# Kernel optimization log

Measured on AMD Instinct MI355X. Metric: run time of the kernel, lower is better.

## Reference

```python
import jax, jax.numpy as jnp
import numpy as np

B, T, IN, HID, BR, OUT = 128, 250, 700, 1024, 4, 20
VTH1, VTH2, DT = 0.5, 0.5, 1.0

# heaviside spike with multi-gaussian surrogate grad (DH-SNN ActFun_adp)
@jax.custom_vjp
def spike_fn(v):
    return (v > 0).astype(v.dtype)

def _spike_fwd(v):
    return spike_fn(v), v

def _spike_bwd(v, g):
    gamma, lens, scale, hight = 0.5, 0.5, 6.0, 0.15
    def gauss(x, mu, sigma):
        return jnp.exp(-((x - mu) ** 2) / (2.0 * sigma ** 2)) / (jnp.sqrt(2.0 * jnp.pi) * sigma)
    sg = (gauss(v, 0.0, lens) * (1.0 + hight)
          - gauss(v, lens, scale * lens) * hight
          - gauss(v, -lens, scale * lens) * hight)
    return (g * sg * gamma,)

spike_fn.defvjp(_spike_fwd, _spike_bwd)

def _make_mask(rng):
    # each output neuron's BR branches see disjoint equal slices of a random permutation
    K = IN + HID  # pad == 0 since (IN+HID) % BR == 0
    seg = K // BR
    mask = np.zeros((HID * BR, K), dtype=np.int32)
    for i in range(HID):
        seq = rng.permutation(K)
        for j in range(BR):
            mask[i * BR + j, seq[j * seg:(j + 1) * seg]] = 1
    return mask

def setup_inputs() -> dict:
    key = jax.random.key(0)
    ks = jax.random.split(key, 10)
    K = IN + HID
    x = jax.random.uniform(ks[0], (B, T, IN), dtype=jnp.float32)
    W1 = jax.random.normal(ks[1], (HID * BR, K), dtype=jnp.float32) / jnp.sqrt(jnp.float32(K))
    b1 = jnp.zeros((HID * BR,), jnp.float32)
    tau_m1 = jax.random.uniform(ks[2], (HID,), jnp.float32, 0.0, 4.0)
    tau_n = jax.random.uniform(ks[3], (HID, BR), jnp.float32, 0.0, 4.0)
    W2 = jax.random.normal(ks[4], (OUT, HID), dtype=jnp.float32) / jnp.sqrt(jnp.float32(HID))
    b2 = jnp.zeros((OUT,), jnp.float32)
    tau_m2 = jax.random.uniform(ks[5], (OUT,), jnp.float32, 0.0, 4.0)
    mem1_0 = jax.random.uniform(ks[6], (B, HID), jnp.float32)
    mem2_0 = jax.random.uniform(ks[7], (B, OUT), jnp.float32)
    mask = jnp.asarray(_make_mask(np.random.default_rng(0)))
    return dict(x=x, W1=W1, b1=b1, tau_m1=tau_m1, tau_n=tau_n, W2=W2, b2=b2,
                tau_m2=tau_m2, mem1_0=mem1_0, mem2_0=mem2_0, mask=mask)

def reference(x, W1, b1, tau_m1, tau_n, W2, b2, tau_m2, mem1_0, mem2_0, mask):
    bsz = x.shape[0]
    W1m = W1 * mask.astype(W1.dtype)  # branch-sparse dendritic weights
    alpha1 = jax.nn.sigmoid(tau_m1)   # [HID]
    beta = jax.nn.sigmoid(tau_n)      # [HID, BR]
    alpha2 = jax.nn.sigmoid(tau_m2)   # [OUT]
    spk1_0 = jnp.zeros((bsz, HID), x.dtype)
    d0 = jnp.zeros((bsz, HID, BR), x.dtype)
    spk2_0 = jnp.zeros((bsz, OUT), x.dtype)

    def step(carry, x_t):
        mem1, spk1, d_inp, mem2, spk2 = carry
        k_in = jnp.concatenate([x_t, spk1], axis=1)          # [B, IN+HID]
        ff = (k_in @ W1m.T + b1).reshape(bsz, HID, BR)       # dendritic branch input
        d_inp = beta * d_inp + (1.0 - beta) * ff             # per-branch decay
        l_in = d_inp.sum(axis=2)                             # [B, HID]
        mem1 = mem1 * alpha1 + (1.0 - alpha1) * l_in - VTH1 * spk1 * DT
        spk1 = spike_fn(mem1 - VTH1)
        d2 = spk1 @ W2.T + b2
        mem2 = mem2 * alpha2 + (1.0 - alpha2) * d2 - VTH2 * spk2 * DT
        spk2 = spike_fn(mem2 - VTH2)
        out = jax.nn.log_softmax(mem2, axis=1)
        return (mem1, spk1, d_inp, mem2, spk2), out

    _, ys = jax.lax.scan(step, (mem1_0, spk1_0, d0, mem2_0, spk2_0), jnp.swapaxes(x, 0, 1))
    return jnp.transpose(ys, (1, 2, 0))  # [B, OUT, T]
```

## Files before the change

kernel.cpp:

```cpp
#include <hip/hip_runtime.h>
#include <stdint.h>

#define BATCH 128
#define TSTEPS 250
#define NIN 700
#define NHID 1024
#define NBR 4
#define NOUT 20
#define KDIM 1724
#define NR 4096
#define VTH 0.5f

typedef float f32x4 __attribute__((ext_vector_type(4)));
typedef short s16x8 __attribute__((ext_vector_type(8)));


__global__ void setup_small(const float* __restrict__ tau_m1, const float* __restrict__ tau_n,
                            const float* __restrict__ tau_m2, const float* __restrict__ W2,
                            float* __restrict__ alpha1, float* __restrict__ beta,
                            float* __restrict__ alpha2, float* __restrict__ W2T) {
    int i = blockIdx.x * blockDim.x + threadIdx.x;
    if (i < NHID)  alpha1[i] = 1.f / (1.f + expf(-tau_m1[i]));
    if (i < NR)    beta[i]   = 1.f / (1.f + expf(-tau_n[i]));
    if (i < 32)    alpha2[i] = (i < NOUT) ? 1.f / (1.f + expf(-tau_m2[i])) : 0.f;
    if (i < NHID * 32) {
        int j = i >> 5, o = i & 31;
        W2T[i] = (o < NOUT) ? W2[o * NHID + j] : 0.f;
    }
}

__device__ __forceinline__ uint16_t f2bf_rne(float x) {
    uint32_t u = __float_as_uint(x);
    return (uint16_t)((u + 0x7FFFu + ((u >> 16) & 1u)) >> 16);
}

__global__ void setup_weights(const float* __restrict__ W1, const int* __restrict__ mask,
                              float* __restrict__ W1xT, uint16_t* __restrict__ fragH,
                              uint16_t* __restrict__ fragL) {
    const int total1 = NIN * NR;
    const int total2 = 128 << 15;
    for (int i = blockIdx.x * blockDim.x + threadIdx.x; i < total1 + total2;
         i += gridDim.x * blockDim.x) {
        if (i < total1) {
            int k = i >> 12, r = i & 4095;
            size_t src = (size_t)r * KDIM + k;
            W1xT[i] = W1[src] * (float)mask[src];
        } else {
            int e = i - total1;
            int j = e & 7, lane = (e >> 3) & 63, ks = (e >> 9) & 31;
            int nt2 = (e >> 14) & 1, gb = e >> 15;
            int k = ks * 32 + ((lane >> 4) & 3) * 8 + j;
            int r = gb * 32 + nt2 * 16 + (lane & 15);
            size_t src = (size_t)r * KDIM + NIN + k;
            float w = W1[src] * (float)mask[src];
            uint16_t hb = f2bf_rne(w);
            float hf = __uint_as_float((uint32_t)hb << 16);
            fragH[e] = hb;
            fragL[e] = f2bf_rne(w - hf);
        }
    }
}

__global__ void init_state(const float* __restrict__ mem1_0, const float* __restrict__ mem2_0,
                           float* __restrict__ mem1, float* __restrict__ mem2,
                           float* __restrict__ spk2, float* __restrict__ d_inp,
                           uint32_t* __restrict__ spkg, uint32_t* __restrict__ bar) {
    int i = blockIdx.x * blockDim.x + threadIdx.x;
    if (i < BATCH * NR) d_inp[i] = 0.f;
    if (i < BATCH * NHID) mem1[i] = mem1_0[i];
    if (i < BATCH * NOUT) { mem2[i] = mem2_0[i]; spk2[i] = 0.f; }
    if (i < 8192) spkg[i] = 0u;
    if (i < 2048) bar[i] = 0u;
}


#define GBM 128
#define GBN 128
#define GBK 16

__global__ __launch_bounds__(256) void ffx_gemm(const float* __restrict__ x,
                                                const float* __restrict__ W1xT,
                                                const float* __restrict__ b1,
                                                float* __restrict__ ffx, int t0) {
    __shared__ float As[GBK][GBM];
    __shared__ float Bs[GBK][GBN];
    int dt = blockIdx.x, bn = blockIdx.y;
    int tid = threadIdx.x;
    int tn = tid & 15, tm = tid >> 4;

    float acc[8][8];
#pragma unroll
    for (int i = 0; i < 8; ++i)
#pragma unroll
        for (int j = 0; j < 8; ++j) acc[i][j] = 0.f;

    int m_l = tid >> 1;
    const float* xrow = x + ((size_t)m_l * TSTEPS + t0 + dt) * NIN;
    int kh = (tid & 1) * 8;
    int kb = tid >> 4;
    int nb = (tid & 15) * 8;

    for (int k0 = 0; k0 < NIN; k0 += GBK) {
        float av[8];
#pragma unroll
        for (int u = 0; u < 8; ++u) {
            int k = k0 + kh + u;
            av[u] = (k < NIN) ? xrow[k] : 0.f;
        }
#pragma unroll
        for (int u = 0; u < 8; ++u) As[kh + u][m_l] = av[u];

        bool kok = (k0 + kb) < NIN;
        const float* bp = W1xT + (size_t)(k0 + kb) * NR + bn * GBN + nb;
        float bv[8];
#pragma unroll
        for (int u = 0; u < 8; ++u) bv[u] = kok ? bp[u] : 0.f;
#pragma unroll
        for (int u = 0; u < 8; ++u) Bs[kb][nb + u] = bv[u];

        __syncthreads();
#pragma unroll
        for (int kk = 0; kk < GBK; ++kk) {
            float a[8], b[8];
#pragma unroll
            for (int u = 0; u < 8; ++u) a[u] = As[kk][tm * 8 + u];
#pragma unroll
            for (int u = 0; u < 8; ++u) b[u] = Bs[kk][tn * 8 + u];
#pragma unroll
            for (int i = 0; i < 8; ++i)
#pragma unroll
                for (int j = 0; j < 8; ++j) acc[i][j] += a[i] * b[j];
        }
        __syncthreads();
    }

    float bias[8];
#pragma unroll
    for (int j = 0; j < 8; ++j) bias[j] = b1[bn * GBN + tn * 8 + j];
#pragma unroll
    for (int i = 0; i < 8; ++i) {
        int brow = tm * 8 + i;
        float* cp = ffx + ((size_t)dt * BATCH + brow) * NR + bn * GBN + tn * 8;
#pragma unroll
        for (int j = 0; j < 8; ++j) cp[j] = acc[i][j] + bias[j];
    }
}


__global__ __launch_bounds__(512) void persist9(
    const float* __restrict__ alpha1, const float* __restrict__ beta,
    const float* __restrict__ alpha2, float* __restrict__ mem1,
    float* __restrict__ mem2, float* __restrict__ spk2,
    float* __restrict__ d_inp, const uint16_t* __restrict__ fragH_g,
    const uint16_t* __restrict__ fragL_g, const float* __restrict__ W2T,
    const float* __restrict__ ffx, const float* __restrict__ b2v,
    float* __restrict__ out, uint32_t* __restrict__ spkg,
    uint32_t* __restrict__ bar, int t0, int tc, int last, int epoch0) {
    __shared__ __align__(16) uint16_t lds_fh[32768];
    __shared__ __align__(16) uint16_t lds_fl[32768];
    __shared__ uint32_t lds_raw[2048];
    __shared__ uint32_t lds_mask[64 * 33];
    __shared__ float lds_part[2560];

    const int blk = blockIdx.x;
    const int tid = threadIdx.x;
    const int G   = blk >> 7;
    const int gb  = blk & 127;
    const int l   = tid & 63;
    const int wv  = tid >> 6;

    {
        const float4* sH = (const float4*)(fragH_g + (size_t)gb * 32768);
        const float4* sL = (const float4*)(fragL_g + (size_t)gb * 32768);
        for (int i4 = tid; i4 < 4096; i4 += 512) {
            ((float4*)lds_fh)[i4] = sH[i4];
            ((float4*)lds_fl)[i4] = sL[i4];
        }
    }

    const int mt  = wv >> 1;
    const int nt2 = wv & 1;
    const int arow = mt * 16 + (l & 15);
    const int ksl  = ((l >> 4) & 3) * 8;

    const int ub = tid >> 3;
    const int un = tid & 7;
    const int bg_ = G * 64 + ub;
    const int n_g = gb * 8 + un;
    const int r0  = gb * 32 + un * 4;
    const f32x4 bet = *(const f32x4*)&beta[r0];
    const float al  = alpha1[n_g];
    f32x4 di = *(const f32x4*)&d_inp[(size_t)bg_ * NR + r0];
    float mm = mem1[bg_ * NHID + n_g];

    const int o2 = tid & 31;
    const int sub = tid >> 5;
    const bool l2blk = (gb < 16) && ((sub & 3) == 0);
    const int b2l = gb * 4 + (sub >> 2);
    const int b2g = G * 64 + b2l;
    float m2 = 0.f, s2v = 0.f, a2 = 0.f, bo = 0.f;
    if (l2blk && o2 < NOUT) {
        a2 = alpha2[o2];
        bo = b2v[o2];
        m2 = mem2[b2g * NOUT + o2];
        s2v = spk2[b2g * NOUT + o2];
    }

    uint32_t* breg = bar + (size_t)G * 1024;
    const int sg = gb & 7;
    uint32_t* grpcnt = &breg[32 * (1 + sg)];
    uint32_t* goline = &breg[32 * (9 + sg)];
    const bool leader = (gb >= 120);

    const int iters = tc + (last ? 1 : 0);
    for (int it = 0; it < iters; ++it) {
        const int tt = t0 + it;

        f32x4 ff = {0.f, 0.f, 0.f, 0.f};
        if (tt < TSTEPS)
            ff = *(const f32x4*)(ffx + (size_t)it * (BATCH * NR) + (size_t)bg_ * NR + r0);

        if (it > 0) {
            if (tid == 0) {
                uint32_t tgt = (uint32_t)(epoch0 + it);
                if (leader) {
                    while (__hip_atomic_load(&breg[0], __ATOMIC_ACQUIRE,
                                             __HIP_MEMORY_SCOPE_AGENT) < 8u * tgt)
                        __builtin_amdgcn_s_sleep(2);
                    __hip_atomic_store(goline, tgt, __ATOMIC_RELEASE,
                                       __HIP_MEMORY_SCOPE_AGENT);
                } else {
                    while (__hip_atomic_load(goline, __ATOMIC_RELAXED,
                                             __HIP_MEMORY_SCOPE_AGENT) < tgt)
                        __builtin_amdgcn_s_sleep(2);
                }
            }
            __syncthreads();
        }

        {
            const uint32_t* spg = spkg + (size_t)((tt + 1) & 1) * 4096 + G * 2048;
#pragma unroll
            for (int k2 = 0; k2 < 4; ++k2) {
                int idx = tid + (k2 << 9);
                lds_raw[idx ^ ((idx >> 6) & 31)] =
                    __hip_atomic_load(&spg[idx], __ATOMIC_RELAXED, __HIP_MEMORY_SCOPE_AGENT);
            }
        }
        __syncthreads();

        {
#pragma unroll
            for (int k2 = 0; k2 < 4; ++k2) {
                int e = tid + (k2 << 9);
                int b = e >> 5, w = e & 31;
                uint32_t word = 0;
#pragma unroll
                for (int m = 0; m < 4; ++m) {
                    int raw = ((w << 2) + m) * 16 + (b >> 2);
                    uint32_t v = lds_raw[raw ^ ((raw >> 6) & 31)];
                    word |= ((v >> ((b & 3) * 8)) & 0xFFu) << (m * 8);
                }
                lds_mask[b * 33 + w] = word;
            }
        }
        __syncthreads();

        if (tt < TSTEPS) {
            f32x4 accH = {0.f, 0.f, 0.f, 0.f};
            f32x4 accL = {0.f, 0.f, 0.f, 0.f};
            const int maskbase = arow * 33;
            const int fbase = nt2 * 32;
#pragma unroll 4
            for (int ks = 0; ks < 32; ++ks) {
                uint32_t bits = (lds_mask[maskbase + ks] >> ksl) & 0xFFu;
                union { uint32_t u[4]; s16x8 v; } a;
                a.u[0] = ((bits & 1u)  ? 0x3F80u : 0u) | ((bits & 2u)   ? 0x3F800000u : 0u);
                a.u[1] = ((bits & 4u)  ? 0x3F80u : 0u) | ((bits & 8u)   ? 0x3F800000u : 0u);
                a.u[2] = ((bits & 16u) ? 0x3F80u : 0u) | ((bits & 32u)  ? 0x3F800000u : 0u);
                a.u[3] = ((bits & 64u) ? 0x3F80u : 0u) | ((bits & 128u) ? 0x3F800000u : 0u);
                const s16x8 bh = *(const s16x8*)&lds_fh[((fbase + ks) * 64 + l) * 8];
                const s16x8 bl = *(const s16x8*)&lds_fl[((fbase + ks) * 64 + l) * 8];
                accH = __builtin_amdgcn_mfma_f32_16x16x32_bf16(a.v, bh, accH, 0, 0, 0);
                accL = __builtin_amdgcn_mfma_f32_16x16x32_bf16(a.v, bl, accL, 0, 0, 0);
            }
            f32x4 d;
#pragma unroll
            for (int q = 0; q < 4; ++q) d[q] = accH[q] + accL[q];
            float* pp = lds_part + ((mt * 32 + nt2 * 16 + (l & 15)) * 20 + ((l >> 4) & 3) * 4);
            *(float4*)pp = *(float4*)&d;
        }
        __syncthreads();

        if (tt < TSTEPS) {
            const int rl0 = un * 4;
            float s[4];
#pragma unroll
            for (int q = 0; q < 4; ++q)
                s[q] = lds_part[((ub >> 4) * 32 + rl0 + q) * 20 + (ub & 15)];
#pragma unroll
            for (int q = 0; q < 4; ++q)
                di[q] = bet[q] * di[q] + (1.f - bet[q]) * (s[q] + ff[q]);
            float lsum = (di[0] + di[1]) + (di[2] + di[3]);
            float sp_prev = (float)((lds_mask[ub * 33 + (n_g >> 5)] >> (n_g & 31)) & 1u);
            float mn = mm * al + (1.f - al) * lsum - VTH * sp_prev;
            mm = mn;
            bool spk = (mn - VTH) > 0.f;
            unsigned long long bal = __ballot(spk);
            uint32_t* spn = spkg + (size_t)(tt & 1) * 4096 + G * 2048;
            if (l == 0)
                __hip_atomic_store(&spn[gb * 16 + wv * 2], (uint32_t)bal,
                                   __ATOMIC_RELAXED, __HIP_MEMORY_SCOPE_AGENT);
            if (l == 32)
                __hip_atomic_store(&spn[gb * 16 + wv * 2 + 1], (uint32_t)(bal >> 32),
                                   __ATOMIC_RELAXED, __HIP_MEMORY_SCOPE_AGENT);
        }

        __syncthreads();
        if (it + 1 < iters && tid == 0) {
            uint32_t e16 = 16u * (uint32_t)(epoch0 + it + 1);
            uint32_t old = __hip_atomic_fetch_add(grpcnt, 1u, __ATOMIC_RELEASE,
                                                  __HIP_MEMORY_SCOPE_AGENT);
            if (old == e16 - 1u)
                __hip_atomic_fetch_add(&breg[0], 1u, __ATOMIC_RELEASE,
                                       __HIP_MEMORY_SCOPE_AGENT);
        }

        if (tt > 0 && l2blk) {
            const uint32_t* mw = &lds_mask[b2l * 33];
            float d2 = bo;
            for (int w = 0; w < 32; ++w) {
                uint32_t bits = mw[w];
                while (bits) {
                    int p = __builtin_ctz(bits);
                    bits &= bits - 1;
                    d2 += W2T[(((w << 5) + p) << 5) + o2];
                }
            }
            float m2n = m2 * a2 + (1.f - a2) * d2 - VTH * s2v;
            m2 = m2n;
            s2v = ((m2n - VTH) > 0.f) ? 1.f : 0.f;
            float v = (o2 < NOUT) ? m2n : -3.4e38f;
#pragma unroll
            for (int off = 16; off >= 1; off >>= 1) v = fmaxf(v, __shfl_xor(v, off, 32));
            float e = (o2 < NOUT) ? expf(m2n - v) : 0.f;
            float ssum = e;
#pragma unroll
            for (int off = 16; off >= 1; off >>= 1) ssum += __shfl_xor(ssum, off, 32);
            if (o2 < NOUT) out[((size_t)b2g * NOUT + o2) * TSTEPS + (tt - 1)] = (m2n - v) - logf(ssum);
        }
    }

    *(f32x4*)&d_inp[(size_t)bg_ * NR + r0] = di;
    mem1[bg_ * NHID + n_g] = mm;
    if (l2blk && o2 < NOUT) {
        mem2[b2g * NOUT + o2] = m2;
        spk2[b2g * NOUT + o2] = s2v;
    }
}


extern "C" void kernel_launch(void* const* d_in, const int* in_sizes, int n_in,
                              void* d_out, int out_size, void* d_ws, size_t ws_size,
                              hipStream_t stream) {
    const float* x      = (const float*)d_in[0];
    const float* W1     = (const float*)d_in[1];
    const float* b1     = (const float*)d_in[2];
    const float* tau_m1 = (const float*)d_in[3];
    const float* tau_n  = (const float*)d_in[4];
    const float* W2     = (const float*)d_in[5];
    const float* b2     = (const float*)d_in[6];
    const float* tau_m2 = (const float*)d_in[7];
    const float* mem1_0 = (const float*)d_in[8];
    const float* mem2_0 = (const float*)d_in[9];
    const int*   mask   = (const int*)d_in[10];
    float* out = (float*)d_out;

    float* ws = (float*)d_ws;
    size_t F = 0;
    float* alpha1 = ws + F; F += 1024;
    float* beta   = ws + F; F += 4096;
    float* alpha2 = ws + F; F += 32;
    float* mem1   = ws + F; F += BATCH * NHID;
    float* mem2   = ws + F; F += BATCH * NOUT;
    float* spk2   = ws + F; F += BATCH * NOUT;
    float* d_inp  = ws + F; F += BATCH * NR;
    float* W1xT   = ws + F; F += (size_t)NIN * NR;
    uint16_t* fragH = (uint16_t*)(ws + F); F += (size_t)(128 << 15) / 2;
    uint16_t* fragL = (uint16_t*)(ws + F); F += (size_t)(128 << 15) / 2;
    float* W2T    = ws + F; F += NHID * 32;
    uint32_t* spkg = (uint32_t*)(ws + F); F += 8192;
    uint32_t* bar  = (uint32_t*)(ws + F); F += 2048;
    float* ffx = ws + F;

    size_t ws_f = ws_size / 4;
    size_t avail = (ws_f > F) ? (ws_f - F) : 0;
    size_t per_t = (size_t)BATCH * NR;
    int Tc = (int)(avail / per_t);
    if (Tc < 1) Tc = 1;
    if (Tc > TSTEPS) Tc = TSTEPS;

    hipLaunchKernelGGL(setup_small, dim3(128), dim3(256), 0, stream,
                       tau_m1, tau_n, tau_m2, W2, alpha1, beta, alpha2, W2T);
    hipLaunchKernelGGL(setup_weights, dim3(2048), dim3(256), 0, stream,
                       W1, mask, W1xT, fragH, fragL);
    hipLaunchKernelGGL(init_state, dim3(2048), dim3(256), 0, stream,
                       mem1_0, mem2_0, mem1, mem2, spk2, d_inp, spkg, bar);

    int chunk_start = 0;
    int barriers_done = 0;
    while (chunk_start < TSTEPS) {
        int tc = TSTEPS - chunk_start;
        if (tc > Tc) tc = Tc;
        int last = (chunk_start + tc >= TSTEPS) ? 1 : 0;

        hipLaunchKernelGGL(ffx_gemm, dim3(tc, 32), dim3(256), 0, stream,
                           x, W1xT, b1, ffx, chunk_start);
        hipLaunchKernelGGL(persist9, dim3(256), dim3(512), 0, stream,
                           alpha1, beta, alpha2, mem1, mem2, spk2, d_inp, fragH, fragL,
                           W2T, ffx, b2, out, spkg, bar, chunk_start, tc, last, barriers_done);

        int iters = tc + (last ? 1 : 0);
        barriers_done += iters - 1;
        chunk_start += tc;
    }
}
```

Baseline: 6.111 ms.

## Replace grid barrier with tagged 64-bit spike words polled per step

Removes the hierarchical atomic-counter grid barrier. Each spike word is now written together with a timestep tag in a 64-bit atomic store, using a 4-deep ring of buffers. Consumers spin on the tag of each word they need, so blocks synchronise only through data readiness instead of a counter plus leader broadcast. The LDS bit-transpose into a mask layout is also dropped, and the raw ballot layout is indexed directly in the MMA and output paths. This removes one barrier round trip per step, at the cost of doubling spike traffic and many threads polling global memory.

```diff
diff --git a/kernel.cpp b/kernel.cpp
--- a/kernel.cpp
+++ b/kernel.cpp
@@ -64,13 +64,12 @@
 __global__ void init_state(const float* __restrict__ mem1_0, const float* __restrict__ mem2_0,
                            float* __restrict__ mem1, float* __restrict__ mem2,
                            float* __restrict__ spk2, float* __restrict__ d_inp,
-                           uint32_t* __restrict__ spkg, uint32_t* __restrict__ bar) {
+                           uint32_t* __restrict__ spk) {
     int i = blockIdx.x * blockDim.x + threadIdx.x;
     if (i < BATCH * NR) d_inp[i] = 0.f;
     if (i < BATCH * NHID) mem1[i] = mem1_0[i];
     if (i < BATCH * NOUT) { mem2[i] = mem2_0[i]; spk2[i] = 0.f; }
-    if (i < 8192) spkg[i] = 0u;
-    if (i < 2048) bar[i] = 0u;
+    if (i < 32768) spk[i] = 0u;
 }
 
 
@@ -147,19 +146,18 @@
 }
 
 
-__global__ __launch_bounds__(512) void persist9(
+__global__ __launch_bounds__(512) void persist10(
     const float* __restrict__ alpha1, const float* __restrict__ beta,
     const float* __restrict__ alpha2, float* __restrict__ mem1,
     float* __restrict__ mem2, float* __restrict__ spk2,
     float* __restrict__ d_inp, const uint16_t* __restrict__ fragH_g,
     const uint16_t* __restrict__ fragL_g, const float* __restrict__ W2T,
     const float* __restrict__ ffx, const float* __restrict__ b2v,
-    float* __restrict__ out, uint32_t* __restrict__ spkg,
-    uint32_t* __restrict__ bar, int t0, int tc, int last, int epoch0) {
+    float* __restrict__ out, uint64_t* __restrict__ spk,
+    int t0, int tc, int last) {
     __shared__ __align__(16) uint16_t lds_fh[32768];
     __shared__ __align__(16) uint16_t lds_fl[32768];
     __shared__ uint32_t lds_raw[2048];
-    __shared__ uint32_t lds_mask[64 * 33];
     __shared__ float lds_part[2560];
 
     const int blk = blockIdx.x;
@@ -182,6 +180,9 @@
     const int nt2 = wv & 1;
     const int arow = mt * 16 + (l & 15);
     const int ksl  = ((l >> 4) & 3) * 8;
+    const int lhi  = (l >> 4) & 3;
+    const int rawoff = arow >> 2;
+    const int ashf   = (arow & 3) * 8;
 
     const int ub = tid >> 3;
     const int un = tid & 7;
@@ -206,12 +207,6 @@
         s2v = spk2[b2g * NOUT + o2];
     }
 
-    uint32_t* breg = bar + (size_t)G * 1024;
-    const int sg = gb & 7;
-    uint32_t* grpcnt = &breg[32 * (1 + sg)];
-    uint32_t* goline = &breg[32 * (9 + sg)];
-    const bool leader = (gb >= 120);
-
     const int iters = tc + (last ? 1 : 0);
     for (int it = 0; it < iters; ++it) {
         const int tt = t0 + it;
@@ -220,60 +215,37 @@
         if (tt < TSTEPS)
             ff = *(const f32x4*)(ffx + (size_t)it * (BATCH * NR) + (size_t)bg_ * NR + r0);
 
-        if (it > 0) {
-            if (tid == 0) {
-                uint32_t tgt = (uint32_t)(epoch0 + it);
-                if (leader) {
-                    while (__hip_atomic_load(&breg[0], __ATOMIC_ACQUIRE,
-                                             __HIP_MEMORY_SCOPE_AGENT) < 8u * tgt)
-                        __builtin_amdgcn_s_sleep(2);
-                    __hip_atomic_store(goline, tgt, __ATOMIC_RELEASE,
-                                       __HIP_MEMORY_SCOPE_AGENT);
-                } else {
-                    while (__hip_atomic_load(goline, __ATOMIC_RELAXED,
-                                             __HIP_MEMORY_SCOPE_AGENT) < tgt)
-                        __builtin_amdgcn_s_sleep(2);
+        __syncthreads();
+
+        {
+            const uint64_t* sp = spk + ((size_t)(tt & 3) * 2 + G) * 2048;
+            const uint32_t tag = (uint32_t)tt;
+            uint64_t v[4];
+#pragma unroll
+            for (int k2 = 0; k2 < 4; ++k2)
+                v[k2] = __hip_atomic_load(&sp[tid + (k2 << 9)], __ATOMIC_RELAXED,
+                                          __HIP_MEMORY_SCOPE_AGENT);
+#pragma unroll
+            for (int k2 = 0; k2 < 4; ++k2) {
+                while ((uint32_t)v[k2] != tag) {
+                    __builtin_amdgcn_s_sleep(1);
+                    v[k2] = __hip_atomic_load(&sp[tid + (k2 << 9)], __ATOMIC_RELAXED,
+                                              __HIP_MEMORY_SCOPE_AGENT);
                 }
             }
-            __syncthreads();
-        }
-
-        {
-            const uint32_t* spg = spkg + (size_t)((tt + 1) & 1) * 4096 + G * 2048;
-#pragma unroll
-            for (int k2 = 0; k2 < 4; ++k2) {
-                int idx = tid + (k2 << 9);
-                lds_raw[idx ^ ((idx >> 6) & 31)] =
-                    __hip_atomic_load(&spg[idx], __ATOMIC_RELAXED, __HIP_MEMORY_SCOPE_AGENT);
-            }
-        }
-        __syncthreads();
-
-        {
-#pragma unroll
-            for (int k2 = 0; k2 < 4; ++k2) {
-                int e = tid + (k2 << 9);
-                int b = e >> 5, w = e & 31;
-                uint32_t word = 0;
-#pragma unroll
-                for (int m = 0; m < 4; ++m) {
-                    int raw = ((w << 2) + m) * 16 + (b >> 2);
-                    uint32_t v = lds_raw[raw ^ ((raw >> 6) & 31)];
-                    word |= ((v >> ((b & 3) * 8)) & 0xFFu) << (m * 8);
-                }
-                lds_mask[b * 33 + w] = word;
-            }
+#pragma unroll
+            for (int k2 = 0; k2 < 4; ++k2)
+                lds_raw[tid + (k2 << 9)] = (uint32_t)(v[k2] >> 32);
         }
         __syncthreads();
 
         if (tt < TSTEPS) {
             f32x4 accH = {0.f, 0.f, 0.f, 0.f};
             f32x4 accL = {0.f, 0.f, 0.f, 0.f};
-            const int maskbase = arow * 33;
             const int fbase = nt2 * 32;
 #pragma unroll 4
             for (int ks = 0; ks < 32; ++ks) {
-                uint32_t bits = (lds_mask[maskbase + ks] >> ksl) & 0xFFu;
+                uint32_t bits = (lds_raw[((ks << 2) + lhi) * 16 + rawoff] >> ashf) & 0xFFu;
                 union { uint32_t u[4]; s16x8 v; } a;
                 a.u[0] = ((bits & 1u)  ? 0x3F80u : 0u) | ((bits & 2u)   ? 0x3F800000u : 0u);
                 a.u[1] = ((bits & 4u)  ? 0x3F80u : 0u) | ((bits & 8u)   ? 0x3F800000u : 0u);
@@ -302,39 +274,33 @@
             for (int q = 0; q < 4; ++q)
                 di[q] = bet[q] * di[q] + (1.f - bet[q]) * (s[q] + ff[q]);
             float lsum = (di[0] + di[1]) + (di[2] + di[3]);
-            float sp_prev = (float)((lds_mask[ub * 33 + (n_g >> 5)] >> (n_g & 31)) & 1u);
+            float sp_prev = (float)((lds_raw[gb * 16 + (ub >> 2)] >> ((ub & 3) * 8 + un)) & 1u);
             float mn = mm * al + (1.f - al) * lsum - VTH * sp_prev;
             mm = mn;
-            bool spk = (mn - VTH) > 0.f;
-            unsigned long long bal = __ballot(spk);
-            uint32_t* spn = spkg + (size_t)(tt & 1) * 4096 + G * 2048;
+            bool spkb = (mn - VTH) > 0.f;
+            unsigned long long bal = __ballot(spkb);
+            uint64_t* spn = spk + ((size_t)((tt + 1) & 3) * 2 + G) * 2048;
+            const uint64_t ntag = (uint64_t)(uint32_t)(tt + 1);
             if (l == 0)
-                __hip_atomic_store(&spn[gb * 16 + wv * 2], (uint32_t)bal,
+                __hip_atomic_store(&spn[gb * 16 + wv * 2],
+                                   ((uint64_t)(uint32_t)bal << 32) | ntag,
                                    __ATOMIC_RELAXED, __HIP_MEMORY_SCOPE_AGENT);
             if (l == 32)
-                __hip_atomic_store(&spn[gb * 16 + wv * 2 + 1], (uint32_t)(bal >> 32),
+                __hip_atomic_store(&spn[gb * 16 + wv * 2 + 1],
+                                   ((uint64_t)(uint32_t)(bal >> 32) << 32) | ntag,
                                    __ATOMIC_RELAXED, __HIP_MEMORY_SCOPE_AGENT);
         }
 
-        __syncthreads();
-        if (it + 1 < iters && tid == 0) {
-            uint32_t e16 = 16u * (uint32_t)(epoch0 + it + 1);
-            uint32_t old = __hip_atomic_fetch_add(grpcnt, 1u, __ATOMIC_RELEASE,
-                                                  __HIP_MEMORY_SCOPE_AGENT);
-            if (old == e16 - 1u)
-                __hip_atomic_fetch_add(&breg[0], 1u, __ATOMIC_RELEASE,
-                                       __HIP_MEMORY_SCOPE_AGENT);
-        }
-
         if (tt > 0 && l2blk) {
-            const uint32_t* mw = &lds_mask[b2l * 33];
+            const int sh2 = (b2l & 3) * 8;
+            const int off2 = b2l >> 2;
             float d2 = bo;
-            for (int w = 0; w < 32; ++w) {
-                uint32_t bits = mw[w];
+            for (int g2 = 0; g2 < 128; ++g2) {
+                uint32_t bits = (lds_raw[g2 * 16 + off2] >> sh2) & 0xFFu;
                 while (bits) {
                     int p = __builtin_ctz(bits);
                     bits &= bits - 1;
-                    d2 += W2T[(((w << 5) + p) << 5) + o2];
+                    d2 += W2T[(((g2 << 3) + p) << 5) + o2];
                 }
             }
             float m2n = m2 * a2 + (1.f - a2) * d2 - VTH * s2v;
@@ -389,8 +355,8 @@
     uint16_t* fragH = (uint16_t*)(ws + F); F += (size_t)(128 << 15) / 2;
     uint16_t* fragL = (uint16_t*)(ws + F); F += (size_t)(128 << 15) / 2;
     float* W2T    = ws + F; F += NHID * 32;
-    uint32_t* spkg = (uint32_t*)(ws + F); F += 8192;
-    uint32_t* bar  = (uint32_t*)(ws + F); F += 2048;
+    F = (F + 1) & ~(size_t)1;
+    uint64_t* spk = (uint64_t*)(ws + F); F += 32768;
     float* ffx = ws + F;
 
     size_t ws_f = ws_size / 4;
@@ -405,10 +371,9 @@
     hipLaunchKernelGGL(setup_weights, dim3(2048), dim3(256), 0, stream,
                        W1, mask, W1xT, fragH, fragL);
     hipLaunchKernelGGL(init_state, dim3(2048), dim3(256), 0, stream,
-                       mem1_0, mem2_0, mem1, mem2, spk2, d_inp, spkg, bar);
+                       mem1_0, mem2_0, mem1, mem2, spk2, d_inp, (uint32_t*)spk);
 
     int chunk_start = 0;
-    int barriers_done = 0;
     while (chunk_start < TSTEPS) {
         int tc = TSTEPS - chunk_start;
         if (tc > Tc) tc = Tc;
@@ -416,12 +381,10 @@
 
         hipLaunchKernelGGL(ffx_gemm, dim3(tc, 32), dim3(256), 0, stream,
                            x, W1xT, b1, ffx, chunk_start);
-        hipLaunchKernelGGL(persist9, dim3(256), dim3(512), 0, stream,
+        hipLaunchKernelGGL(persist10, dim3(256), dim3(512), 0, stream,
                            alpha1, beta, alpha2, mem1, mem2, spk2, d_inp, fragH, fragL,
-                           W2T, ffx, b2, out, spkg, bar, chunk_start, tc, last, barriers_done);
-
-        int iters = tc + (last ? 1 : 0);
-        barriers_done += iters - 1;
+                           W2T, ffx, b2, out, spk, chunk_start, tc, last);
+
         chunk_start += tc;
     }
 }
```

Result: slower. 6.352 ms (+3.9%).
